# Performance work log

Measured on AMD Instinct MI355X. Metric: run time of the kernel, lower is better.

Reference implementation:

```python
import jax, jax.numpy as jnp
import numpy as np

N_NODES = 50000
DEG = 32
N_EDGES = N_NODES * DEG
NODE_FT_DIM = 64  # hardcoded in original forward
ALPHA = 0.2


def setup_inputs() -> dict:
    key = jax.random.key(0)
    ks = jax.random.split(key, 8)
    node_fts = jax.random.normal(ks[0], (N_NODES, 256), dtype=jnp.float32)
    edge_fts = jax.random.normal(ks[1], (N_EDGES, 32), dtype=jnp.float32)
    # edges sorted by source, fixed degree -> matches original repeat_interleave semantics
    src = jnp.repeat(jnp.arange(N_NODES, dtype=jnp.int64), DEG)
    dst = jax.random.randint(ks[2], (N_EDGES,), 0, N_NODES, dtype=jnp.int64)
    edges = jnp.stack([src, dst], axis=1)
    W_node = jax.random.normal(ks[3], (256, 64), dtype=jnp.float32) * 0.06
    W_edge = jax.random.normal(ks[4], (32, 64), dtype=jnp.float32) * 0.14
    a_node = jax.random.normal(ks[5], (128, 1), dtype=jnp.float32) * 0.12
    a_edge = jax.random.normal(ks[6], (128, 1), dtype=jnp.float32) * 0.12
    return {"node_fts": node_fts, "edge_fts": edge_fts, "edges": edges,
            "W_node": W_node, "W_edge": W_edge, "a_node": a_node, "a_edge": a_edge}


def _leaky(x):
    return jnp.where(x >= 0, x, ALPHA * x)


def reference(node_fts, edge_fts, edges, W_node, W_edge, a_node, a_edge):
    n_nodes = node_fts.shape[0]
    src, dst = edges[:, 0], edges[:, 1]
    edge_fts_padded = jnp.pad(edge_fts, ((0, 0), (0, NODE_FT_DIM - edge_fts.shape[1])))

    h_v = node_fts @ W_node   # [N, 64]
    e_v = edge_fts @ W_edge   # [E, 64]

    # attention logits: [h_src || h_dst] @ a_node == h@a1 gathered + h@a2 gathered
    a_n1, a_n2 = a_node[:NODE_FT_DIM, 0], a_node[NODE_FT_DIM:, 0]
    a_e1, a_e2 = a_edge[:NODE_FT_DIM, 0], a_edge[NODE_FT_DIM:, 0]
    node_att = _leaky((h_v @ a_n1)[src] + (h_v @ a_n2)[dst])          # [E]
    # edge branch replaces slot 1 with padded edge features
    edge_att = _leaky((h_v @ a_e1)[src] + edge_fts_padded @ a_e2)      # [E]

    def seg_softmax(att):
        w = jnp.exp(jnp.clip(att, -2.0, 2.0))
        denom = jax.ops.segment_sum(w, src, num_segments=n_nodes)
        return w / denom[src]

    node_att_norm = seg_softmax(node_att)
    edge_att_norm = seg_softmax(edge_att)
    node_att_var = jnp.var(node_att_norm, ddof=1)
    edge_att_var = jnp.var(edge_att_norm, ddof=1)

    node_out = jax.ops.segment_sum(h_v[dst] * node_att_norm[:, None], src, num_segments=n_nodes)
    # original indexes e_v (per-edge rows) with node indices dst; in-range since E > N
    edge_out = jax.ops.segment_sum(e_v[dst] * edge_att_norm[:, None], src, num_segments=n_nodes)
    return node_out, edge_out, node_att_var, edge_att_var
```

## Files before the change

kernel.cpp:

```cpp
#include <hip/hip_runtime.h>
#include <hip/hip_fp16.h>

#define ALPHA 0.2f
static constexpr int NN = 50000;
static constexpr long NE = (long)NN * 32;

static constexpr long WS_HN1 = 0;
static constexpr long WS_HN2 = NN;
static constexpr long WS_HE1 = 2L * NN;
static constexpr long WS_ST  = 3L * NN;
static constexpr long WS_P   = 5L * NN;
static constexpr long WS_HEV = 5L * NN + 512;

__global__ __launch_bounds__(256) void k_hv(const float* __restrict__ A,
                                            const float* __restrict__ W,
                                            const float* __restrict__ a_node,
                                            const float* __restrict__ a_edge,
                                            __half* __restrict__ hev,
                                            float* __restrict__ hn1,
                                            float* __restrict__ hn2,
                                            float* __restrict__ he1) {
    __shared__ float As[16][65];
    __shared__ float Ws[16][64];
    const int t  = threadIdx.x;
    const int m0 = blockIdx.x * 64;
    const int tr = t >> 4, tc = t & 15;
    const int lr = t >> 2, seg = t & 3;
    const int wk = t >> 4, wc = t & 15;

    float acc[4][4] = {};
    for (int k0 = 0; k0 < 256; k0 += 16) {
        int row = m0 + lr;
        float4 av = make_float4(0.f, 0.f, 0.f, 0.f);
        if (row < NN)
            av = *reinterpret_cast<const float4*>(&A[(long)row * 256 + k0 + seg * 4]);
        As[seg*4+0][lr] = av.x; As[seg*4+1][lr] = av.y;
        As[seg*4+2][lr] = av.z; As[seg*4+3][lr] = av.w;
        *reinterpret_cast<float4*>(&Ws[wk][wc*4]) =
            *reinterpret_cast<const float4*>(&W[(k0 + wk) * 64 + wc * 4]);
        __syncthreads();
        #pragma unroll
        for (int kk = 0; kk < 16; ++kk) {
            float a0 = As[kk][tr*4+0], a1 = As[kk][tr*4+1];
            float a2 = As[kk][tr*4+2], a3 = As[kk][tr*4+3];
            float b0 = Ws[kk][tc*4+0], b1 = Ws[kk][tc*4+1];
            float b2 = Ws[kk][tc*4+2], b3 = Ws[kk][tc*4+3];
            acc[0][0] += a0*b0; acc[0][1] += a0*b1; acc[0][2] += a0*b2; acc[0][3] += a0*b3;
            acc[1][0] += a1*b0; acc[1][1] += a1*b1; acc[1][2] += a1*b2; acc[1][3] += a1*b3;
            acc[2][0] += a2*b0; acc[2][1] += a2*b1; acc[2][2] += a2*b2; acc[2][3] += a2*b3;
            acc[3][0] += a3*b0; acc[3][1] += a3*b1; acc[3][2] += a3*b2; acc[3][3] += a3*b3;
        }
        __syncthreads();
    }

    float an1[4], an2[4], ae1[4];
    #pragma unroll
    for (int j = 0; j < 4; ++j) {
        an1[j] = a_node[tc*4 + j];
        an2[j] = a_node[64 + tc*4 + j];
        ae1[j] = a_edge[tc*4 + j];
    }

    #pragma unroll
    for (int q = 0; q < 4; ++q) {
        float p1 = 0.f, p2 = 0.f, p3 = 0.f;
        #pragma unroll
        for (int j = 0; j < 4; ++j) {
            p1 += acc[q][j] * an1[j];
            p2 += acc[q][j] * an2[j];
            p3 += acc[q][j] * ae1[j];
        }
        #pragma unroll
        for (int m = 1; m <= 8; m <<= 1) {
            p1 += __shfl_xor(p1, m);
            p2 += __shfl_xor(p2, m);
            p3 += __shfl_xor(p3, m);
        }
        int row = m0 + tr * 4 + q;
        if (row < NN) {
            ushort4 hp;
            hp.x = __half_as_ushort(__float2half(acc[q][0]));
            hp.y = __half_as_ushort(__float2half(acc[q][1]));
            hp.z = __half_as_ushort(__float2half(acc[q][2]));
            hp.w = __half_as_ushort(__float2half(acc[q][3]));
            *reinterpret_cast<ushort4*>(&hev[(long)row * 128 + tc * 4]) = hp;
            if (tc == 0) { hn1[row] = p1; hn2[row] = p2; he1[row] = p3; }
        }
    }
}

__global__ __launch_bounds__(256) void k_ev(const float* __restrict__ ef,
                                            const float* __restrict__ We,
                                            __half* __restrict__ hev) {
    const int lane = threadIdx.x & 63, w = threadIdx.x >> 6;
    const int r = blockIdx.x * 4 + w;
    float acc = 0.f;
    #pragma unroll
    for (int k = 0; k < 32; ++k)
        acc += ef[(long)r * 32 + k] * We[k * 64 + lane];
    hev[(long)r * 128 + 64 + lane] = __float2half(acc);
}

__global__ __launch_bounds__(256) void k_edge(const float* __restrict__ ef,
                                              const int*   __restrict__ edges,
                                              const float* __restrict__ a_edge,
                                              const float* __restrict__ hn1,
                                              const float* __restrict__ hn2,
                                              const float* __restrict__ he1,
                                              const __half* __restrict__ hev,
                                              float* __restrict__ st,
                                              float* __restrict__ out) {
    const int t = threadIdx.x;
    const int w = t >> 6, l = t & 63;
    const int n = blockIdx.x * 4 + w;
    const int i = l >> 1, h = l & 1;
    const long ebase = (long)n * 32;

    const int d = edges[(ebase + i) * 2 + 1];

    const float4* efb = reinterpret_cast<const float4*>(&ef[(ebase + i) * 32 + h * 16]);
    float4 v0 = efb[0], v1 = efb[1], v2 = efb[2], v3 = efb[3];

    __half2 h2[32];
    #pragma unroll
    for (int u = 0; u < 32; ++u) {
        int du = __builtin_amdgcn_readlane(d, 2 * u);
        h2[u] = *reinterpret_cast<const __half2*>(&hev[(long)du * 128 + l * 2]);
    }

    float dot;
    {
        const float* ae = &a_edge[64 + h * 16];
        float4 a0q = *reinterpret_cast<const float4*>(ae);
        float4 a1q = *reinterpret_cast<const float4*>(ae + 4);
        float4 a2q = *reinterpret_cast<const float4*>(ae + 8);
        float4 a3q = *reinterpret_cast<const float4*>(ae + 12);
        dot = v0.x*a0q.x + v0.y*a0q.y + v0.z*a0q.z + v0.w*a0q.w
            + v1.x*a1q.x + v1.y*a1q.y + v1.z*a1q.z + v1.w*a1q.w
            + v2.x*a2q.x + v2.y*a2q.y + v2.z*a2q.z + v2.w*a2q.w
            + v3.x*a3q.x + v3.y*a3q.y + v3.z*a3q.z + v3.w*a3q.w;
    }
    dot += __shfl_xor(dot, 1);

    float attn = hn1[n] + hn2[d];
    attn = attn >= 0.f ? attn : ALPHA * attn;
    float wn = __expf(fminf(fmaxf(attn, -2.f), 2.f));

    float atte = he1[n] + dot;
    atte = atte >= 0.f ? atte : ALPHA * atte;
    float we = __expf(fminf(fmaxf(atte, -2.f), 2.f));

    float dn = wn, de = we;
    #pragma unroll
    for (int m = 2; m <= 32; m <<= 1) { dn += __shfl_xor(dn, m); de += __shfl_xor(de, m); }
    float nn = wn / dn, ne = we / de;

    float sqn = nn * nn, sqe = ne * ne;
    #pragma unroll
    for (int m = 2; m <= 32; m <<= 1) { sqn += __shfl_xor(sqn, m); sqe += __shfl_xor(sqe, m); }
    if (l == 0) { st[n] = sqn; st[NN + n] = sqe; }

    __half2 wpk = __floats2half2_rn(nn, ne);
    unsigned int wbits = *reinterpret_cast<unsigned int*>(&wpk);

    const bool isE = l >= 32;
    float a0 = 0.f, a1 = 0.f;
    #pragma unroll
    for (int u = 0; u < 32; ++u) {
        unsigned int wv = (unsigned int)__builtin_amdgcn_readlane((int)wbits, 2 * u);
        __half2 wp = *reinterpret_cast<__half2*>(&wv);
        float wt = isE ? __high2float(wp) : __low2float(wp);
        float2 f = __half22float2(h2[u]);
        a0 = fmaf(wt, f.x, a0);
        a1 = fmaf(wt, f.y, a1);
    }
    long off = isE ? ((long)NN * 64 + (long)n * 64 + (l - 32) * 2)
                   : ((long)n * 64 + l * 2);
    *reinterpret_cast<float2*>(&out[off]) = make_float2(a0, a1);
}

__global__ __launch_bounds__(256) void k_red1(const float* __restrict__ st,
                                              float* __restrict__ part) {
    const int t = threadIdx.x;
    const int n = blockIdx.x * 256 + t;
    float v0 = 0.f, v1 = 0.f;
    if (n < NN) { v0 = st[n]; v1 = st[NN + n]; }
    #pragma unroll
    for (int m = 1; m <= 32; m <<= 1) { v0 += __shfl_xor(v0, m); v1 += __shfl_xor(v1, m); }
    __shared__ float ls[4][2];
    const int wv = t >> 6;
    if ((t & 63) == 0) { ls[wv][0] = v0; ls[wv][1] = v1; }
    __syncthreads();
    if (t == 0) {
        part[(long)blockIdx.x * 2]     = ls[0][0] + ls[1][0] + ls[2][0] + ls[3][0];
        part[(long)blockIdx.x * 2 + 1] = ls[0][1] + ls[1][1] + ls[2][1] + ls[3][1];
    }
}

__global__ __launch_bounds__(64) void k_red2(const float* __restrict__ part,
                                             float* __restrict__ out) {
    const int t = threadIdx.x;
    double v0 = 0.0, v1 = 0.0;
    for (int b = t; b < 196; b += 64) {
        v0 += (double)part[b * 2];
        v1 += (double)part[b * 2 + 1];
    }
    #pragma unroll
    for (int m = 1; m <= 32; m <<= 1) { v0 += __shfl_xor(v0, m); v1 += __shfl_xor(v1, m); }
    if (t == 0) {
        const double M = (double)NE;
        const double corr = (double)NN * (double)NN / M;
        out[6400000] = (float)((v0 - corr) / (M - 1.0));
        out[6400001] = (float)((v1 - corr) / (M - 1.0));
    }
}

extern "C" void kernel_launch(void* const* d_in, const int* in_sizes, int n_in,
                              void* d_out, int out_size, void* d_ws, size_t ws_size,
                              hipStream_t stream) {
    const float* node_fts = (const float*)d_in[0];
    const float* edge_fts = (const float*)d_in[1];
    const int*   edges    = (const int*)  d_in[2];
    const float* W_node   = (const float*)d_in[3];
    const float* W_edge   = (const float*)d_in[4];
    const float* a_node   = (const float*)d_in[5];
    const float* a_edge   = (const float*)d_in[6];
    float* out = (float*)d_out;
    float* ws  = (float*)d_ws;

    float*  hn1 = ws + WS_HN1;
    float*  hn2 = ws + WS_HN2;
    float*  he1 = ws + WS_HE1;
    float*  st  = ws + WS_ST;
    float*  prt = ws + WS_P;
    __half* hev = (__half*)(ws + WS_HEV);

    k_hv  <<<(NN + 63) / 64, 256, 0, stream>>>(node_fts, W_node, a_node, a_edge,
                                               hev, hn1, hn2, he1);
    k_ev  <<<NN / 4, 256, 0, stream>>>(edge_fts, W_edge, hev);
    k_edge<<<NN / 4, 256, 0, stream>>>(edge_fts, edges, a_edge, hn1, hn2, he1,
                                       hev, st, out);
    k_red1<<<196, 256, 0, stream>>>(st, prt);
    k_red2<<<1, 64, 0, stream>>>(prt, out);
}
```

Measured before the change: 166.5 us.

## Tile hev gathers by destination range and use nontemporal streaming loads/stores

Splits the gather of hev rows into four destination-index ranges, loading only the rows whose dst falls in the current range and accumulating them before moving on. Each step also issues the loads for the next range ahead of the accumulation. The intent is to improve L2 locality of the random gathers and overlap loads with compute. Edge features, edge indices and outputs now use nontemporal loads and stores so they do not pollute the cache. The cost is uniform-per-lane branching, repeated readlanes and more scalar control flow. Because the warp-level gathers are already fully issued in one pass before, the tiling may add serialization.

```diff
diff --git a/kernel.cpp b/kernel.cpp
--- a/kernel.cpp
+++ b/kernel.cpp
@@ -4,13 +4,18 @@
 #define ALPHA 0.2f
 static constexpr int NN = 50000;
 static constexpr long NE = (long)NN * 32;
+static constexpr int TILES = 4;
+static constexpr int TILE_N = NN / TILES;
+
+typedef float f4v __attribute__((ext_vector_type(4)));
+typedef float f2v __attribute__((ext_vector_type(2)));
 
 static constexpr long WS_HN1 = 0;
 static constexpr long WS_HN2 = NN;
 static constexpr long WS_HE1 = 2L * NN;
 static constexpr long WS_ST  = 3L * NN;
 static constexpr long WS_P   = 5L * NN;
-static constexpr long WS_HEV = 5L * NN + 512;
+static constexpr long WS_HEV = 250560;
 
 __global__ __launch_bounds__(256) void k_hv(const float* __restrict__ A,
                                             const float* __restrict__ W,
@@ -116,16 +121,20 @@
     const int i = l >> 1, h = l & 1;
     const long ebase = (long)n * 32;
 
-    const int d = edges[(ebase + i) * 2 + 1];
-
-    const float4* efb = reinterpret_cast<const float4*>(&ef[(ebase + i) * 32 + h * 16]);
-    float4 v0 = efb[0], v1 = efb[1], v2 = efb[2], v3 = efb[3];
+    const int d = __builtin_nontemporal_load(&edges[(ebase + i) * 2 + 1]);
+
+    const f4v* efb = reinterpret_cast<const f4v*>(&ef[(ebase + i) * 32 + h * 16]);
+    f4v v0 = __builtin_nontemporal_load(efb + 0);
+    f4v v1 = __builtin_nontemporal_load(efb + 1);
+    f4v v2 = __builtin_nontemporal_load(efb + 2);
+    f4v v3 = __builtin_nontemporal_load(efb + 3);
 
     __half2 h2[32];
     #pragma unroll
     for (int u = 0; u < 32; ++u) {
         int du = __builtin_amdgcn_readlane(d, 2 * u);
-        h2[u] = *reinterpret_cast<const __half2*>(&hev[(long)du * 128 + l * 2]);
+        if (du < TILE_N)
+            h2[u] = *reinterpret_cast<const __half2*>(&hev[(long)du * 128 + l * 2]);
     }
 
     float dot;
@@ -166,17 +175,35 @@
     const bool isE = l >= 32;
     float a0 = 0.f, a1 = 0.f;
     #pragma unroll
-    for (int u = 0; u < 32; ++u) {
-        unsigned int wv = (unsigned int)__builtin_amdgcn_readlane((int)wbits, 2 * u);
-        __half2 wp = *reinterpret_cast<__half2*>(&wv);
-        float wt = isE ? __high2float(wp) : __low2float(wp);
-        float2 f = __half22float2(h2[u]);
-        a0 = fmaf(wt, f.x, a0);
-        a1 = fmaf(wt, f.y, a1);
-    }
+    for (int tile = 0; tile < TILES; ++tile) {
+        if (tile + 1 < TILES) {
+            const int lo = (tile + 1) * TILE_N, hi = lo + TILE_N;
+            #pragma unroll
+            for (int u = 0; u < 32; ++u) {
+                int du = __builtin_amdgcn_readlane(d, 2 * u);
+                if (du >= lo && du < hi)
+                    h2[u] = *reinterpret_cast<const __half2*>(&hev[(long)du * 128 + l * 2]);
+            }
+        }
+        const int lo = tile * TILE_N, hi = lo + TILE_N;
+        #pragma unroll
+        for (int u = 0; u < 32; ++u) {
+            int du = __builtin_amdgcn_readlane(d, 2 * u);
+            if (du >= lo && du < hi) {
+                unsigned int wv = (unsigned int)__builtin_amdgcn_readlane((int)wbits, 2 * u);
+                __half2 wp = *reinterpret_cast<__half2*>(&wv);
+                float wt = isE ? __high2float(wp) : __low2float(wp);
+                float2 f = __half22float2(h2[u]);
+                a0 = fmaf(wt, f.x, a0);
+                a1 = fmaf(wt, f.y, a1);
+            }
+        }
+    }
+
     long off = isE ? ((long)NN * 64 + (long)n * 64 + (l - 32) * 2)
                    : ((long)n * 64 + l * 2);
-    *reinterpret_cast<float2*>(&out[off]) = make_float2(a0, a1);
+    f2v o; o.x = a0; o.y = a1;
+    __builtin_nontemporal_store(o, reinterpret_cast<f2v*>(&out[off]));
 }
 
 __global__ __launch_bounds__(256) void k_red1(const float* __restrict__ st,
```

Result: slower. 197.9 us (+18.8%).
